# Performance work log

Hardware: AMD Instinct MI355X
Metric: run time of the kernel (lower is better)

Reference implementation:

```python
import jax, jax.numpy as jnp
import numpy as np
from jax import lax
import math

KS = 7  # attention kernel size
PAD = 3


def conv2d(x, w, b, pad):
    y = lax.conv_general_dilated(x, w, (1, 1), [(pad, pad), (pad, pad)],
                                 dimension_numbers=('NCHW', 'OIHW', 'NCHW'))
    return y + b[None, :, None, None]


def unfold(x):
    # x: [B, C, H, W] -> [B, C, KS*KS, H, W], matching nn.Unfold channel-major order
    B, C, H, W = x.shape
    xp = jnp.pad(x, ((0, 0), (0, 0), (PAD, PAD), (PAD, PAD)))
    patches = [xp[:, :, i:i + H, j:j + W] for i in range(KS) for j in range(KS)]
    return jnp.stack(patches, axis=2)


def setup_inputs() -> dict:
    key = jax.random.key(0)
    ks = jax.random.split(key, 12)
    B, H, W = 1, 256, 256
    s = lambda fan: 1.0 / np.sqrt(fan)
    inp = {
        'x': jax.random.normal(ks[0], (B, 6, H, W), jnp.float32),
        'w0': jax.random.normal(ks[1], (48, 3, 3, 3), jnp.float32) * s(3 * 9),
        'b0': jnp.zeros((48,), jnp.float32),
        'w1': jax.random.normal(ks[2], (48, 48, 3, 3), jnp.float32) * s(48 * 9),
        'b1': jnp.zeros((48,), jnp.float32),
        'w2': jax.random.normal(ks[3], (48, 48, 3, 3), jnp.float32) * s(48 * 9),
        'b2': jnp.zeros((48,), jnp.float32),
        'w3': jax.random.normal(ks[4], (24, 48, 3, 3), jnp.float32) * s(48 * 9),
        'b3': jnp.zeros((24,), jnp.float32),
        'skip_w': jax.random.normal(ks[5], (24, 3, 1, 1), jnp.float32) * s(3),
        'skip_b': jnp.zeros((24,), jnp.float32),
        'q_w': jax.random.normal(ks[6], (24, 24, 1, 1), jnp.float32) * s(24),
        'q_b': jnp.zeros((24,), jnp.float32),
        'k_w': jax.random.normal(ks[7], (24, 24, 1, 1), jnp.float32) * s(24),
        'k_b': jnp.zeros((24,), jnp.float32),
        'v_w': jax.random.normal(ks[8], (24, 24, 1, 1), jnp.float32) * s(24),
        'v_b': jnp.zeros((24,), jnp.float32),
    }
    return inp


def reference(x, w0, b0, w1, b1, w2, b2, w3, b3, skip_w, skip_b,
              q_w, q_b, k_w, k_b, v_w, v_b):
    def submodel(t):
        h = jax.nn.relu(conv2d(t, w0, b0, 1))
        h = jax.nn.relu(conv2d(h, w1, b1, 1))
        h = jax.nn.relu(conv2d(h, w2, b2, 1))
        h = jax.nn.relu(conv2d(h, w3, b3, 1))
        return h + conv2d(t, skip_w, skip_b, 0)

    xa, xb = jnp.split(x, 2, axis=1)  # [B,3,H,W] each
    a = submodel(xa)                  # [B,24,H,W]
    b = submodel(xb)

    Q = conv2d(b, q_w, q_b, 0)        # [B,24,H,W]
    K = unfold(conv2d(a, k_w, k_b, 0))  # [B,24,49,H,W]
    V = unfold(conv2d(a, v_w, v_b, 0))  # [B,24,49,H,W]

    C = Q.shape[1]
    A = jnp.einsum('bchw,bcphw->bphw', Q, K) / math.sqrt(C)
    A = jax.nn.softmax(A, axis=1)     # softmax over 49 local positions
    y = jnp.einsum('bphw,bcphw->bchw', A, V)
    return jnp.concatenate([y + a, b], axis=1)  # [B,48,H,W]
```

## Files before the change

kernel.cpp:

```cpp
#include <hip/hip_runtime.h>
#include <math.h>

#define HH 256
#define WW 256
#define NN (HH * WW)

typedef _Float16 f16;
typedef _Float16 f16x8 __attribute__((ext_vector_type(8)));
typedef _Float16 f16x4 __attribute__((ext_vector_type(4)));
typedef float f32x4 __attribute__((ext_vector_type(4)));

__global__ __launch_bounds__(256) void xh_convert(const float* __restrict__ x,
                                                  f16* __restrict__ xh) {
  int p = blockIdx.x * 256 + threadIdx.x;
  int z = p >= NN;
  int q = p - z * NN;
  const float* xz = x + (size_t)z * 3 * NN;
  f16x4 v;
  v[0] = (f16)xz[q];
  v[1] = (f16)xz[NN + q];
  v[2] = (f16)xz[2 * NN + q];
  v[3] = (f16)0.f;
  *(f16x4*)(xh + (size_t)p * 4) = v;
}

__global__ __launch_bounds__(256) void repack_frags(
    const float* __restrict__ w0, const float* __restrict__ w1,
    const float* __restrict__ w2, const float* __restrict__ w3,
    const float* __restrict__ qw, const float* __restrict__ kw,
    const float* __restrict__ vw, f16* __restrict__ bf) {
  const int O1 = 1536, O2 = O1 + 27648, O3 = O2 + 27648, OQ = O3 + 18432;
  int e = blockIdx.x * 256 + threadIdx.x;
  if (e >= OQ + 3072) return;
  float val = 0.f;
  if (e >= OQ) {
    int idx = e - OQ;
    int mat = idx >> 10;
    int r = idx & 1023;
    int nt = r >> 9;
    int lane = (r >> 3) & 63;
    int j = r & 7;
    int n = lane & 15, quad = lane >> 4;
    int ci = quad * 8 + j, co = nt * 16 + n;
    const float* w = (mat == 0) ? qw : (mat == 1) ? kw : vw;
    if (ci < 24 && co < 24) val = w[co * 24 + ci];
  } else {
    const float* w;
    int COUT, idx, mode;
    if (e < O1)      { w = w0; COUT = 48; idx = e;      mode = 0; }
    else if (e < O2) { w = w1; COUT = 48; idx = e - O1; mode = 1; }
    else if (e < O3) { w = w2; COUT = 48; idx = e - O2; mode = 1; }
    else             { w = w3; COUT = 24; idx = e - O3; mode = 1; }
    int j = idx & 7;
    int lane = (idx >> 3) & 63;
    int rest = idx >> 9;
    int n = lane & 15, quad = lane >> 4;
    if (mode == 0) {
      int nt = rest;
      int k = quad * 8 + j;
      int cout = nt * 16 + n;
      if (k < 27) {
        int tap = k / 3, ci = k - tap * 3;
        val = w[(cout * 3 + ci) * 9 + tap];
      }
    } else {
      int kc = rest & 1;
      int tap = (rest >> 1) % 9;
      int nt = (rest >> 1) / 9;
      int ci = kc * 32 + quad * 8 + j;
      int cout = nt * 16 + n;
      if (ci < 48 && cout < COUT) val = w[(cout * 48 + ci) * 9 + tap];
    }
  }
  bf[e] = (f16)val;
}

__global__ __launch_bounds__(256, 2) void conv0_gemm(
    const f16* __restrict__ xh, const f16* __restrict__ bf0,
    const float* __restrict__ bias, f16* __restrict__ outh) {
  extern __shared__ char smem[];
  const int tid = threadIdx.x;
  const int lane = tid & 63, wave = tid >> 6;
  const int n = lane & 15, quad = lane >> 4;
  const int bx = blockIdx.x * 16, by = blockIdx.y * 16, z = blockIdx.z;
  const f16* xz = xh + (size_t)z * NN * 4;

  {
    int p = tid, y = p >> 4, xcol = p & 15;
    int gy = by + y, gx = bx + xcol;
    f16* row = (f16*)(smem + p * 80);
#pragma unroll
    for (int tap = 0; tap < 9; ++tap) {
      int dy = tap / 3, dx = tap - (tap / 3) * 3;
      int sy = gy + dy - 1, sx = gx + dx - 1;
      f16 c0 = (f16)0.f, c1 = c0, c2 = c0;
      if (sy >= 0 && sy < HH && sx >= 0 && sx < WW) {
        const f16* s = xz + ((size_t)sy * WW + sx) * 4;
        c0 = s[0]; c1 = s[1]; c2 = s[2];
      }
      row[tap * 3 + 0] = c0;
      row[tap * 3 + 1] = c1;
      row[tap * 3 + 2] = c2;
    }
#pragma unroll
    for (int k = 27; k < 32; ++k) row[k] = (f16)0.f;
  }
  __syncthreads();

  f32x4 acc[4][3];
#pragma unroll
  for (int nt = 0; nt < 3; ++nt) {
    float bv = bias[nt * 16 + n];
#pragma unroll
    for (int i = 0; i < 4; ++i) acc[i][nt] = (f32x4){bv, bv, bv, bv};
  }
  f16x8 B[3];
#pragma unroll
  for (int nt = 0; nt < 3; ++nt)
    B[nt] = *(const f16x8*)(bf0 + (nt * 64 + lane) * 8);
#pragma unroll
  for (int i = 0; i < 4; ++i) {
    int r = wave * 4 + i;
    f16x8 a = *(const f16x8*)(smem + (r * 16 + n) * 80 + quad * 16);
#pragma unroll
    for (int nt = 0; nt < 3; ++nt)
      acc[i][nt] =
          __builtin_amdgcn_mfma_f32_16x16x32_f16(a, B[nt], acc[i][nt], 0, 0, 0);
  }

  f16* oz = outh + (size_t)z * NN * 48;
#pragma unroll
  for (int i = 0; i < 4; ++i) {
    int y = by + wave * 4 + i;
#pragma unroll
    for (int nt = 0; nt < 3; ++nt)
#pragma unroll
      for (int reg = 0; reg < 4; ++reg)
        oz[((size_t)y * WW + bx + quad * 4 + reg) * 48 + nt * 16 + n] =
            (f16)fmaxf(acc[i][nt][reg], 0.f);
  }
}

template <int NT, int COUT, bool FUSE>
__global__ __launch_bounds__(256, 2) void gemm_conv(
    const f16* __restrict__ in, const f16* __restrict__ bfr,
    const float* __restrict__ bias, f16* __restrict__ outh,
    const float* __restrict__ xsrc, const float* __restrict__ skw,
    const float* __restrict__ skb) {
  extern __shared__ char smem[];
  float* xt = (float*)(smem + 324 * 144);
  const int tid = threadIdx.x;
  const int lane = tid & 63, wave = tid >> 6;
  const int n = lane & 15, quad = lane >> 4;
  const int bx = blockIdx.x * 16, by = blockIdx.y * 16, z = blockIdx.z;
  const f16* inz = in + (size_t)z * NN * 48;

  for (int p = tid; p < 324; p += 256) {
    int yy = p / 18, xx = p - yy * 18;
    int gy = by + yy - 1, gx = bx + xx - 1;
    float4* dst = (float4*)(smem + p * 144);
    if (gy >= 0 && gy < HH && gx >= 0 && gx < WW) {
      const float4* s = (const float4*)(inz + ((size_t)gy * WW + gx) * 48);
      float4 a0 = s[0], a1 = s[1], a2 = s[2], a3 = s[3], a4 = s[4], a5 = s[5];
      dst[0] = a0; dst[1] = a1; dst[2] = a2;
      dst[3] = a3; dst[4] = a4; dst[5] = a5;
      dst[6] = make_float4(0, 0, 0, 0);
      dst[7] = make_float4(0, 0, 0, 0);
    } else {
      float4 zz = make_float4(0, 0, 0, 0);
#pragma unroll
      for (int c = 0; c < 8; ++c) dst[c] = zz;
    }
  }
  if (FUSE) {
    for (int i = tid; i < 768; i += 256) {
      int c = i >> 8, p = i & 255;
      xt[i] = xsrc[(size_t)z * 3 * NN + c * NN + (by + (p >> 4)) * WW + bx +
                   (p & 15)];
    }
  }
  __syncthreads();

  f32x4 acc[4][NT];
#pragma unroll
  for (int nt = 0; nt < NT; ++nt) {
    int cc = nt * 16 + n;
    float bv = (cc < COUT) ? bias[cc] : 0.f;
#pragma unroll
    for (int i = 0; i < 4; ++i) acc[i][nt] = (f32x4){bv, bv, bv, bv};
  }

  const int r0 = wave * 4;
#pragma unroll
  for (int tap = 0; tap < 9; ++tap) {
    const int dy = tap / 3, dx = tap - dy * 3;
    f16x8 B[2][NT];
#pragma unroll
    for (int kc = 0; kc < 2; ++kc)
#pragma unroll
      for (int nt = 0; nt < NT; ++nt)
        B[kc][nt] =
            *(const f16x8*)(bfr + (((nt * 9 + tap) * 2 + kc) * 64 + lane) * 8);
#pragma unroll
    for (int i = 0; i < 4; ++i) {
      const int p = (r0 + i + dy) * 18 + (n + dx);
      const char* ap = smem + p * 144;
      f16x8 a0 = *(const f16x8*)(ap + quad * 16);
      f16x8 a1 = *(const f16x8*)(ap + 64 + quad * 16);
#pragma unroll
      for (int nt = 0; nt < NT; ++nt)
        acc[i][nt] = __builtin_amdgcn_mfma_f32_16x16x32_f16(a0, B[0][nt],
                                                            acc[i][nt], 0, 0, 0);
#pragma unroll
      for (int nt = 0; nt < NT; ++nt)
        acc[i][nt] = __builtin_amdgcn_mfma_f32_16x16x32_f16(a1, B[1][nt],
                                                            acc[i][nt], 0, 0, 0);
    }
  }

  if (!FUSE) {
    f16* oz = outh + (size_t)z * NN * 48;
#pragma unroll
    for (int i = 0; i < 4; ++i) {
      int y = by + r0 + i;
#pragma unroll
      for (int nt = 0; nt < NT; ++nt)
#pragma unroll
        for (int reg = 0; reg < 4; ++reg)
          oz[((size_t)y * WW + bx + quad * 4 + reg) * 48 + nt * 16 + n] =
              (f16)fmaxf(acc[i][nt][reg], 0.f);
    }
  } else {
    f16* oz = outh + (size_t)z * NN * 32;
#pragma unroll
    for (int i = 0; i < 4; ++i) {
      int y = by + r0 + i;
#pragma unroll
      for (int nt = 0; nt < NT; ++nt) {
        int cc = nt * 16 + n;
        float s0 = 0.f, s1 = 0.f, s2 = 0.f, sb0 = 0.f;
        if (cc < 24) {
          s0 = skw[cc * 3 + 0];
          s1 = skw[cc * 3 + 1];
          s2 = skw[cc * 3 + 2];
          sb0 = skb[cc];
        }
#pragma unroll
        for (int reg = 0; reg < 4; ++reg) {
          float v = 0.f;
          if (cc < 24) {
            int pl = (r0 + i) * 16 + quad * 4 + reg;
            float sk = sb0 + s0 * xt[pl] + s1 * xt[256 + pl] + s2 * xt[512 + pl];
            v = fmaxf(acc[i][nt][reg], 0.f) + sk;
          }
          oz[((size_t)(y * WW + bx + quad * 4 + reg)) * 32 + cc] = (f16)v;
        }
      }
    }
  }
}

__global__ __launch_bounds__(256) void qkv_mfma(
    const f16* __restrict__ ABh, const f16* __restrict__ bf,
    const float* __restrict__ qb, const float* __restrict__ kb,
    const float* __restrict__ vb, f16* __restrict__ Qh,
    f16* __restrict__ KVh) {
  const int OQ = 75264;
  const int tid = threadIdx.x;
  const int lane = tid & 63, wave = tid >> 6;
  const int n = lane & 15, quad = lane >> 4;
  const int z = blockIdx.y;
  const f16* src = ABh + (size_t)z * NN * 32;

  if (z == 1) {
    f16x8 QF[2];
#pragma unroll
    for (int nt = 0; nt < 2; ++nt)
      QF[nt] = *(const f16x8*)(bf + OQ + (nt * 64 + lane) * 8);
    float qbias[2];
#pragma unroll
    for (int nt = 0; nt < 2; ++nt) {
      int cc = nt * 16 + n;
      qbias[nt] = (cc < 24) ? qb[cc] : 0.f;
    }
#pragma unroll
    for (int t = 0; t < 4; ++t) {
      int T = blockIdx.x * 16 + wave * 4 + t;
      size_t p0 = (size_t)T * 16;
      f16x8 a8 = *(const f16x8*)(src + p0 * 32 + n * 32 + quad * 8);
#pragma unroll
      for (int nt = 0; nt < 2; ++nt) {
        f32x4 acc = {qbias[nt], qbias[nt], qbias[nt], qbias[nt]};
        acc = __builtin_amdgcn_mfma_f32_16x16x32_f16(a8, QF[nt], acc, 0, 0, 0);
        int cc = nt * 16 + n;
        if (cc < 24) {
#pragma unroll
          for (int reg = 0; reg < 4; ++reg)
            Qh[(p0 + quad * 4 + reg) * 24 + cc] = (f16)acc[reg];
        }
      }
    }
  } else {
    f16x8 KF[2], VF[2];
#pragma unroll
    for (int nt = 0; nt < 2; ++nt) {
      KF[nt] = *(const f16x8*)(bf + OQ + 1024 + (nt * 64 + lane) * 8);
      VF[nt] = *(const f16x8*)(bf + OQ + 2048 + (nt * 64 + lane) * 8);
    }
    float kbias[2], vbias[2];
#pragma unroll
    for (int nt = 0; nt < 2; ++nt) {
      int cc = nt * 16 + n;
      kbias[nt] = (cc < 24) ? kb[cc] : 0.f;
      vbias[nt] = (cc < 24) ? vb[cc] : 0.f;
    }
#pragma unroll
    for (int t = 0; t < 4; ++t) {
      int T = blockIdx.x * 16 + wave * 4 + t;
      size_t p0 = (size_t)T * 16;
      f16x8 a8 = *(const f16x8*)(src + p0 * 32 + n * 32 + quad * 8);
#pragma unroll
      for (int nt = 0; nt < 2; ++nt) {
        f32x4 ak = {kbias[nt], kbias[nt], kbias[nt], kbias[nt]};
        f32x4 av = {vbias[nt], vbias[nt], vbias[nt], vbias[nt]};
        ak = __builtin_amdgcn_mfma_f32_16x16x32_f16(a8, KF[nt], ak, 0, 0, 0);
        av = __builtin_amdgcn_mfma_f32_16x16x32_f16(a8, VF[nt], av, 0, 0, 0);
        int cc = nt * 16 + n;
        if (cc < 24) {
#pragma unroll
          for (int reg = 0; reg < 4; ++reg) {
            KVh[(p0 + quad * 4 + reg) * 48 + cc] = (f16)ak[reg];
            KVh[(p0 + quad * 4 + reg) * 48 + 24 + cc] = (f16)av[reg];
          }
        }
      }
    }
  }
}

__device__ inline float dot8p(f16x8 a, f16x8 b, float acc) {
#if __has_builtin(__builtin_amdgcn_fdot2)
  acc = __builtin_amdgcn_fdot2(__builtin_shufflevector(a, a, 0, 1),
                               __builtin_shufflevector(b, b, 0, 1), acc, false);
  acc = __builtin_amdgcn_fdot2(__builtin_shufflevector(a, a, 2, 3),
                               __builtin_shufflevector(b, b, 2, 3), acc, false);
  acc = __builtin_amdgcn_fdot2(__builtin_shufflevector(a, a, 4, 5),
                               __builtin_shufflevector(b, b, 4, 5), acc, false);
  acc = __builtin_amdgcn_fdot2(__builtin_shufflevector(a, a, 6, 7),
                               __builtin_shufflevector(b, b, 6, 7), acc, false);
  return acc;
#else
#pragma unroll
  for (int i = 0; i < 8; ++i) acc += (float)a[i] * (float)b[i];
  return acc;
#endif
}

__global__ __launch_bounds__(256, 3) void attn_kernel(
    const f16* __restrict__ Qh, const f16* __restrict__ KVh,
    const f16* __restrict__ ABh, float* __restrict__ out) {
  extern __shared__ f16 kv[];
  const int tid = threadIdx.x;
  const int bx = blockIdx.x * 32, by = blockIdx.y * 8;
  const int xl = tid & 31, yl = tid >> 5;
  const int p = (by + yl) * WW + bx + xl;

  f16x8 q0 = *(const f16x8*)(Qh + (size_t)p * 24);
  f16x8 q1 = *(const f16x8*)(Qh + (size_t)p * 24 + 8);
  f16x8 q2 = *(const f16x8*)(Qh + (size_t)p * 24 + 16);

  for (int idx = tid; idx < 3192; idx += 256) {
    int row = idx / 228;
    int rem = idx - row * 228;
    int pxl = rem / 6;
    int c = rem - pxl * 6;
    int gy = by + row - 3, gx = bx + pxl - 3;
    f16x8 v = {};
    if (gy >= 0 && gy < HH && gx >= 0 && gx < WW)
      v = *(const f16x8*)(KVh + ((size_t)(gy * WW + gx)) * 48 + c * 8);
    *(f16x8*)(kv + (row * 38 + pxl) * 56 + c * 8) = v;
  }
  __syncthreads();

  float s[49];
#pragma unroll
  for (int pp = 0; pp < 49; ++pp) {
    int dy = pp / 7, dx = pp - dy * 7;
    const f16* base = kv + ((yl + dy) * 38 + xl + dx) * 56;
    f16x8 k0 = *(const f16x8*)(base);
    f16x8 k1 = *(const f16x8*)(base + 8);
    f16x8 k2 = *(const f16x8*)(base + 16);
    float d = 0.f;
    d = dot8p(q0, k0, d);
    d = dot8p(q1, k1, d);
    d = dot8p(q2, k2, d);
    s[pp] = d * 0.20412414523193154f;
  }

  float m = s[0];
#pragma unroll
  for (int pp = 1; pp < 49; ++pp) m = fmaxf(m, s[pp]);
  float den = 0.f;
#pragma unroll
  for (int pp = 0; pp < 49; ++pp) {
    float e = __expf(s[pp] - m);
    s[pp] = e;
    den += e;
  }
  const float inv = 1.f / den;

  f16x8 y0 = {}, y1 = {}, y2 = {};
#pragma unroll
  for (int pp = 0; pp < 49; ++pp) {
    int dy = pp / 7, dx = pp - dy * 7;
    const f16* base = kv + ((yl + dy) * 38 + xl + dx) * 56 + 24;
    f16 wh = (f16)(s[pp] * inv);
    f16x8 w8 = {wh, wh, wh, wh, wh, wh, wh, wh};
    f16x8 v0 = *(const f16x8*)(base);
    f16x8 v1 = *(const f16x8*)(base + 8);
    f16x8 v2 = *(const f16x8*)(base + 16);
    y0 = v0 * w8 + y0;
    y1 = v1 * w8 + y1;
    y2 = v2 * w8 + y2;
  }

  const f16* ah = ABh + (size_t)p * 32;
  const f16* bh = ABh + (size_t)NN * 32 + (size_t)p * 32;
  f16x8 a0 = *(const f16x8*)(ah);
  f16x8 a1 = *(const f16x8*)(ah + 8);
  f16x8 a2 = *(const f16x8*)(ah + 16);
  f16x8 b0 = *(const f16x8*)(bh);
  f16x8 b1 = *(const f16x8*)(bh + 8);
  f16x8 b2 = *(const f16x8*)(bh + 16);
#pragma unroll
  for (int c = 0; c < 8; ++c) {
    out[(size_t)c * NN + p] = (float)y0[c] + (float)a0[c];
    out[(size_t)(8 + c) * NN + p] = (float)y1[c] + (float)a1[c];
    out[(size_t)(16 + c) * NN + p] = (float)y2[c] + (float)a2[c];
    out[(size_t)(24 + c) * NN + p] = (float)b0[c];
    out[(size_t)(32 + c) * NN + p] = (float)b1[c];
    out[(size_t)(40 + c) * NN + p] = (float)b2[c];
  }
}

extern "C" void kernel_launch(void* const* d_in, const int* in_sizes, int n_in,
                              void* d_out, int out_size, void* d_ws,
                              size_t ws_size, hipStream_t stream) {
  const float* x = (const float*)d_in[0];
  const float* w0 = (const float*)d_in[1];
  const float* b0 = (const float*)d_in[2];
  const float* w1 = (const float*)d_in[3];
  const float* b1 = (const float*)d_in[4];
  const float* w2 = (const float*)d_in[5];
  const float* b2 = (const float*)d_in[6];
  const float* w3 = (const float*)d_in[7];
  const float* b3 = (const float*)d_in[8];
  const float* sw = (const float*)d_in[9];
  const float* sb = (const float*)d_in[10];
  const float* qw = (const float*)d_in[11];
  const float* qb = (const float*)d_in[12];
  const float* kw = (const float*)d_in[13];
  const float* kb = (const float*)d_in[14];
  const float* vw = (const float*)d_in[15];
  const float* vb = (const float*)d_in[16];
  float* out = (float*)d_out;
  float* ws = (float*)d_ws;

  f16* Qh = (f16*)(ws);
  f16* KVh = (f16*)(ws + (size_t)12 * NN);
  f16* ABh = (f16*)(ws + (size_t)36 * NN);
  f16* ACT0 = (f16*)(ws + (size_t)68 * NN);
  f16* ACT1 = (f16*)(ws + (size_t)116 * NN);
  f16* XH = (f16*)(ws + (size_t)164 * NN);
  f16* BF = (f16*)(ws + (size_t)168 * NN);

  xh_convert<<<dim3(512), dim3(256), 0, stream>>>(x, XH);
  repack_frags<<<dim3(306), dim3(256), 0, stream>>>(w0, w1, w2, w3, qw, kw, vw,
                                                    BF);

  dim3 cgrd(16, 16, 2);
  conv0_gemm<<<cgrd, dim3(256), 256 * 80, stream>>>(XH, BF, b0, ACT0);
  gemm_conv<3, 48, false><<<cgrd, dim3(256), 324 * 144, stream>>>(
      ACT0, BF + 1536, b1, ACT1, nullptr, nullptr, nullptr);
  gemm_conv<3, 48, false><<<cgrd, dim3(256), 324 * 144, stream>>>(
      ACT1, BF + 29184, b2, ACT0, nullptr, nullptr, nullptr);
  gemm_conv<2, 24, true><<<cgrd, dim3(256), 324 * 144 + 3072, stream>>>(
      ACT0, BF + 56832, b3, ABh, x, sw, sb);

  qkv_mfma<<<dim3(256, 2), dim3(256), 0, stream>>>(ABh, BF, qb, kb, vb, Qh,
                                                   KVh);

  attn_kernel<<<dim3(8, 32), dim3(256), 532 * 112, stream>>>(Qh, KVh, ABh, out);
}
```

Before: 159.3 us.

## Fuse K/V projection into attention kernel and merge prep kernels

Moves the 1x1 K and V projections into the attention kernel. Each block now loads its halo of the 'a' activations into shared memory and runs MFMA in place to produce K/V, so the KVh buffer is no longer written to or read from global memory. The input conversion and weight repack kernels are merged into one launch, and the residual 'a' values now come from shared memory. The cost is recomputing K/V on halo pixels, extra barriers and a larger shared-memory footprint in the attention kernel.

```diff
diff --git a/kernel.cpp b/kernel.cpp
--- a/kernel.cpp
+++ b/kernel.cpp
@@ -10,27 +10,29 @@
 typedef _Float16 f16x4 __attribute__((ext_vector_type(4)));
 typedef float f32x4 __attribute__((ext_vector_type(4)));
 
-__global__ __launch_bounds__(256) void xh_convert(const float* __restrict__ x,
-                                                  f16* __restrict__ xh) {
-  int p = blockIdx.x * 256 + threadIdx.x;
-  int z = p >= NN;
-  int q = p - z * NN;
-  const float* xz = x + (size_t)z * 3 * NN;
-  f16x4 v;
-  v[0] = (f16)xz[q];
-  v[1] = (f16)xz[NN + q];
-  v[2] = (f16)xz[2 * NN + q];
-  v[3] = (f16)0.f;
-  *(f16x4*)(xh + (size_t)p * 4) = v;
-}
-
-__global__ __launch_bounds__(256) void repack_frags(
-    const float* __restrict__ w0, const float* __restrict__ w1,
-    const float* __restrict__ w2, const float* __restrict__ w3,
-    const float* __restrict__ qw, const float* __restrict__ kw,
-    const float* __restrict__ vw, f16* __restrict__ bf) {
-  const int O1 = 1536, O2 = O1 + 27648, O3 = O2 + 27648, OQ = O3 + 18432;
-  int e = blockIdx.x * 256 + threadIdx.x;
+#define OQ 75264
+
+__global__ __launch_bounds__(256) void prep_kernel(
+    const float* __restrict__ x, const float* __restrict__ w0,
+    const float* __restrict__ w1, const float* __restrict__ w2,
+    const float* __restrict__ w3, const float* __restrict__ qw,
+    const float* __restrict__ kw, const float* __restrict__ vw,
+    f16* __restrict__ xh, f16* __restrict__ bf) {
+  if (blockIdx.x < 512) {
+    int p = blockIdx.x * 256 + threadIdx.x;
+    int z = p >= NN;
+    int q = p - z * NN;
+    const float* xz = x + (size_t)z * 3 * NN;
+    f16x4 v;
+    v[0] = (f16)xz[q];
+    v[1] = (f16)xz[NN + q];
+    v[2] = (f16)xz[2 * NN + q];
+    v[3] = (f16)0.f;
+    *(f16x4*)(xh + (size_t)p * 4) = v;
+    return;
+  }
+  const int O1 = 1536, O2 = O1 + 27648, O3 = O2 + 27648;
+  int e = (blockIdx.x - 512) * 256 + threadIdx.x;
   if (e >= OQ + 3072) return;
   float val = 0.f;
   if (e >= OQ) {
@@ -260,79 +262,38 @@
   }
 }
 
-__global__ __launch_bounds__(256) void qkv_mfma(
-    const f16* __restrict__ ABh, const f16* __restrict__ bf,
-    const float* __restrict__ qb, const float* __restrict__ kb,
-    const float* __restrict__ vb, f16* __restrict__ Qh,
-    f16* __restrict__ KVh) {
-  const int OQ = 75264;
+__global__ __launch_bounds__(256) void q_mfma(const f16* __restrict__ ABh,
+                                              const f16* __restrict__ bf,
+                                              const float* __restrict__ qb,
+                                              f16* __restrict__ Qh) {
   const int tid = threadIdx.x;
   const int lane = tid & 63, wave = tid >> 6;
   const int n = lane & 15, quad = lane >> 4;
-  const int z = blockIdx.y;
-  const f16* src = ABh + (size_t)z * NN * 32;
-
-  if (z == 1) {
-    f16x8 QF[2];
-#pragma unroll
-    for (int nt = 0; nt < 2; ++nt)
-      QF[nt] = *(const f16x8*)(bf + OQ + (nt * 64 + lane) * 8);
-    float qbias[2];
+  const f16* src = ABh + (size_t)NN * 32;
+  f16x8 QF[2];
+#pragma unroll
+  for (int nt = 0; nt < 2; ++nt)
+    QF[nt] = *(const f16x8*)(bf + OQ + (nt * 64 + lane) * 8);
+  float qbias[2];
+#pragma unroll
+  for (int nt = 0; nt < 2; ++nt) {
+    int cc = nt * 16 + n;
+    qbias[nt] = (cc < 24) ? qb[cc] : 0.f;
+  }
+#pragma unroll
+  for (int t = 0; t < 4; ++t) {
+    int T = blockIdx.x * 16 + wave * 4 + t;
+    size_t p0 = (size_t)T * 16;
+    f16x8 a8 = *(const f16x8*)(src + p0 * 32 + n * 32 + quad * 8);
 #pragma unroll
     for (int nt = 0; nt < 2; ++nt) {
+      f32x4 acc = {qbias[nt], qbias[nt], qbias[nt], qbias[nt]};
+      acc = __builtin_amdgcn_mfma_f32_16x16x32_f16(a8, QF[nt], acc, 0, 0, 0);
       int cc = nt * 16 + n;
-      qbias[nt] = (cc < 24) ? qb[cc] : 0.f;
-    }
-#pragma unroll
-    for (int t = 0; t < 4; ++t) {
-      int T = blockIdx.x * 16 + wave * 4 + t;
-      size_t p0 = (size_t)T * 16;
-      f16x8 a8 = *(const f16x8*)(src + p0 * 32 + n * 32 + quad * 8);
-#pragma unroll
-      for (int nt = 0; nt < 2; ++nt) {
-        f32x4 acc = {qbias[nt], qbias[nt], qbias[nt], qbias[nt]};
-        acc = __builtin_amdgcn_mfma_f32_16x16x32_f16(a8, QF[nt], acc, 0, 0, 0);
-        int cc = nt * 16 + n;
-        if (cc < 24) {
-#pragma unroll
-          for (int reg = 0; reg < 4; ++reg)
-            Qh[(p0 + quad * 4 + reg) * 24 + cc] = (f16)acc[reg];
-        }
-      }
-    }
-  } else {
-    f16x8 KF[2], VF[2];
-#pragma unroll
-    for (int nt = 0; nt < 2; ++nt) {
-      KF[nt] = *(const f16x8*)(bf + OQ + 1024 + (nt * 64 + lane) * 8);
-      VF[nt] = *(const f16x8*)(bf + OQ + 2048 + (nt * 64 + lane) * 8);
-    }
-    float kbias[2], vbias[2];
-#pragma unroll
-    for (int nt = 0; nt < 2; ++nt) {
-      int cc = nt * 16 + n;
-      kbias[nt] = (cc < 24) ? kb[cc] : 0.f;
-      vbias[nt] = (cc < 24) ? vb[cc] : 0.f;
-    }
-#pragma unroll
-    for (int t = 0; t < 4; ++t) {
-      int T = blockIdx.x * 16 + wave * 4 + t;
-      size_t p0 = (size_t)T * 16;
-      f16x8 a8 = *(const f16x8*)(src + p0 * 32 + n * 32 + quad * 8);
-#pragma unroll
-      for (int nt = 0; nt < 2; ++nt) {
-        f32x4 ak = {kbias[nt], kbias[nt], kbias[nt], kbias[nt]};
-        f32x4 av = {vbias[nt], vbias[nt], vbias[nt], vbias[nt]};
-        ak = __builtin_amdgcn_mfma_f32_16x16x32_f16(a8, KF[nt], ak, 0, 0, 0);
-        av = __builtin_amdgcn_mfma_f32_16x16x32_f16(a8, VF[nt], av, 0, 0, 0);
-        int cc = nt * 16 + n;
-        if (cc < 24) {
-#pragma unroll
-          for (int reg = 0; reg < 4; ++reg) {
-            KVh[(p0 + quad * 4 + reg) * 48 + cc] = (f16)ak[reg];
-            KVh[(p0 + quad * 4 + reg) * 48 + 24 + cc] = (f16)av[reg];
-          }
-        }
+      if (cc < 24) {
+#pragma unroll
+        for (int reg = 0; reg < 4; ++reg)
+          Qh[(p0 + quad * 4 + reg) * 24 + cc] = (f16)acc[reg];
       }
     }
   }
@@ -357,28 +318,75 @@
 }
 
 __global__ __launch_bounds__(256, 3) void attn_kernel(
-    const f16* __restrict__ Qh, const f16* __restrict__ KVh,
-    const f16* __restrict__ ABh, float* __restrict__ out) {
+    const f16* __restrict__ Qh, const f16* __restrict__ ABh,
+    const f16* __restrict__ bf, const float* __restrict__ kb,
+    const float* __restrict__ vb, float* __restrict__ out) {
   extern __shared__ f16 kv[];
   const int tid = threadIdx.x;
+  const int lane = tid & 63, wave = tid >> 6;
+  const int n16 = lane & 15, quad = lane >> 4;
   const int bx = blockIdx.x * 32, by = blockIdx.y * 8;
   const int xl = tid & 31, yl = tid >> 5;
   const int p = (by + yl) * WW + bx + xl;
+  const f16* ah = ABh;
+  const f16* bh = ABh + (size_t)NN * 32;
 
   f16x8 q0 = *(const f16x8*)(Qh + (size_t)p * 24);
   f16x8 q1 = *(const f16x8*)(Qh + (size_t)p * 24 + 8);
   f16x8 q2 = *(const f16x8*)(Qh + (size_t)p * 24 + 16);
 
-  for (int idx = tid; idx < 3192; idx += 256) {
-    int row = idx / 228;
-    int rem = idx - row * 228;
-    int pxl = rem / 6;
-    int c = rem - pxl * 6;
+  for (int idx = tid; idx < 2128; idx += 256) {
+    int row = idx / 152;
+    int rem = idx - row * 152;
+    int pxl = rem >> 2;
+    int c = rem & 3;
     int gy = by + row - 3, gx = bx + pxl - 3;
     f16x8 v = {};
     if (gy >= 0 && gy < HH && gx >= 0 && gx < WW)
-      v = *(const f16x8*)(KVh + ((size_t)(gy * WW + gx)) * 48 + c * 8);
+      v = *(const f16x8*)(ah + ((size_t)(gy * WW + gx)) * 32 + c * 8);
     *(f16x8*)(kv + (row * 38 + pxl) * 56 + c * 8) = v;
+  }
+  __syncthreads();
+
+  const f16* cs = kv + ((yl + 3) * 38 + xl + 3) * 56;
+  f16x8 a0 = *(const f16x8*)(cs);
+  f16x8 a1 = *(const f16x8*)(cs + 8);
+  f16x8 a2 = *(const f16x8*)(cs + 16);
+  __syncthreads();
+
+  {
+    f16x8 KF[2], VF[2];
+#pragma unroll
+    for (int nt = 0; nt < 2; ++nt) {
+      KF[nt] = *(const f16x8*)(bf + OQ + 1024 + (nt * 64 + lane) * 8);
+      VF[nt] = *(const f16x8*)(bf + OQ + 2048 + (nt * 64 + lane) * 8);
+    }
+    float kbias[2], vbias[2];
+#pragma unroll
+    for (int nt = 0; nt < 2; ++nt) {
+      int cc = nt * 16 + n16;
+      kbias[nt] = (cc < 24) ? kb[cc] : 0.f;
+      vbias[nt] = (cc < 24) ? vb[cc] : 0.f;
+    }
+    for (int t = wave; t < 34; t += 4) {
+      f16x8 a8 = *(const f16x8*)(kv + (t * 16 + n16) * 56 + quad * 8);
+#pragma unroll
+      for (int nt = 0; nt < 2; ++nt) {
+        f32x4 ak = {kbias[nt], kbias[nt], kbias[nt], kbias[nt]};
+        f32x4 av = {vbias[nt], vbias[nt], vbias[nt], vbias[nt]};
+        ak = __builtin_amdgcn_mfma_f32_16x16x32_f16(a8, KF[nt], ak, 0, 0, 0);
+        av = __builtin_amdgcn_mfma_f32_16x16x32_f16(a8, VF[nt], av, 0, 0, 0);
+        int cc = nt * 16 + n16;
+        if (cc < 24) {
+#pragma unroll
+          for (int reg = 0; reg < 4; ++reg) {
+            f16* slot = kv + (t * 16 + quad * 4 + reg) * 56;
+            slot[cc] = (f16)ak[reg];
+            slot[24 + cc] = (f16)av[reg];
+          }
+        }
+      }
+    }
   }
   __syncthreads();
 
@@ -424,14 +432,9 @@
     y2 = v2 * w8 + y2;
   }
 
-  const f16* ah = ABh + (size_t)p * 32;
-  const f16* bh = ABh + (size_t)NN * 32 + (size_t)p * 32;
-  f16x8 a0 = *(const f16x8*)(ah);
-  f16x8 a1 = *(const f16x8*)(ah + 8);
-  f16x8 a2 = *(const f16x8*)(ah + 16);
-  f16x8 b0 = *(const f16x8*)(bh);
-  f16x8 b1 = *(const f16x8*)(bh + 8);
-  f16x8 b2 = *(const f16x8*)(bh + 16);
+  f16x8 b0 = *(const f16x8*)(bh + (size_t)p * 32);
+  f16x8 b1 = *(const f16x8*)(bh + (size_t)p * 32 + 8);
+  f16x8 b2 = *(const f16x8*)(bh + (size_t)p * 32 + 16);
 #pragma unroll
   for (int c = 0; c < 8; ++c) {
     out[(size_t)c * NN + p] = (float)y0[c] + (float)a0[c];
@@ -467,16 +470,14 @@
   float* ws = (float*)d_ws;
 
   f16* Qh = (f16*)(ws);
-  f16* KVh = (f16*)(ws + (size_t)12 * NN);
-  f16* ABh = (f16*)(ws + (size_t)36 * NN);
-  f16* ACT0 = (f16*)(ws + (size_t)68 * NN);
-  f16* ACT1 = (f16*)(ws + (size_t)116 * NN);
-  f16* XH = (f16*)(ws + (size_t)164 * NN);
-  f16* BF = (f16*)(ws + (size_t)168 * NN);
-
-  xh_convert<<<dim3(512), dim3(256), 0, stream>>>(x, XH);
-  repack_frags<<<dim3(306), dim3(256), 0, stream>>>(w0, w1, w2, w3, qw, kw, vw,
-                                                    BF);
+  f16* ABh = (f16*)(ws + (size_t)12 * NN);
+  f16* ACT0 = (f16*)(ws + (size_t)44 * NN);
+  f16* ACT1 = (f16*)(ws + (size_t)92 * NN);
+  f16* XH = (f16*)(ws + (size_t)140 * NN);
+  f16* BF = (f16*)(ws + (size_t)144 * NN);
+
+  prep_kernel<<<dim3(818), dim3(256), 0, stream>>>(x, w0, w1, w2, w3, qw, kw,
+                                                   vw, XH, BF);
 
   dim3 cgrd(16, 16, 2);
   conv0_gemm<<<cgrd, dim3(256), 256 * 80, stream>>>(XH, BF, b0, ACT0);
@@ -487,8 +488,8 @@
   gemm_conv<2, 24, true><<<cgrd, dim3(256), 324 * 144 + 3072, stream>>>(
       ACT0, BF + 56832, b3, ABh, x, sw, sb);
 
-  qkv_mfma<<<dim3(256, 2), dim3(256), 0, stream>>>(ABh, BF, qb, kb, vb, Qh,
-                                                   KVh);
-
-  attn_kernel<<<dim3(8, 32), dim3(256), 532 * 112, stream>>>(Qh, KVh, ABh, out);
-}
+  q_mfma<<<dim3(256), dim3(256), 0, stream>>>(ABh, BF, qb, Qh);
+
+  attn_kernel<<<dim3(8, 32), dim3(256), 544 * 112, stream>>>(Qh, ABh, BF, kb,
+                                                             vb, out);
+}
```

Result: faster. 155.4 us (-2.4%).
